# Kernel tuning notes

Measured on AMD Instinct MI355X. Metric: run time of the kernel, lower is better.

Reference implementation:

```python
import jax, jax.numpy as jnp
import numpy as np

N = 100000
E = 1600000
D = 128

def setup_inputs() -> dict:
    key = jax.random.key(0)
    ks = jax.random.split(key, 12)
    s = 1.0 / np.sqrt(D)
    inp = {
        "x": jax.random.normal(ks[0], (N, D), dtype=jnp.float32),
        "edge_index": jax.random.randint(ks[1], (2, E), 0, N, dtype=jnp.int64),
    }
    names = ["Wl1", "bl1", "Wr1", "Wl2", "bl2", "Wr2", "Wl3", "bl3", "Wr3"]
    shapes = [(D, D), (D,), (D, D)] * 3
    for i, (nm, sh) in enumerate(zip(names, shapes)):
        inp[nm] = jax.random.uniform(ks[2 + i], sh, dtype=jnp.float32, minval=-s, maxval=s)
    return inp


def _sage(x, src, dst, Wl, bl, Wr):
    # messages: gather source node features per edge  [E, D]
    msg = x[src]
    agg = jax.ops.segment_sum(msg, dst, num_segments=x.shape[0])  # [N, D]
    cnt = jax.ops.segment_sum(jnp.ones((src.shape[0], 1), x.dtype), dst,
                              num_segments=x.shape[0])            # [N, 1]
    mean = agg / jnp.maximum(cnt, 1.0)
    # PyG SAGEConv: lin_l(mean_neighbors) + lin_r(self); lin_l has bias
    return mean @ Wl.T + bl + x @ Wr.T


def reference(x, edge_index, Wl1, bl1, Wr1, Wl2, bl2, Wr2, Wl3, bl3, Wr3):
    src, dst = edge_index[0], edge_index[1]
    h = jax.nn.relu(_sage(x, src, dst, Wl1, bl1, Wr1))
    h = jax.nn.relu(_sage(h, src, dst, Wl2, bl2, Wr2))
    h = jax.nn.relu(_sage(h, src, dst, Wl3, bl3, Wr3))
    return h
```

## Files before the change

kernel.cpp:

```cpp
#include <hip/hip_runtime.h>
#include <hip/hip_bf16.h>


#define D 128
#define PAD 48
#define NB_SHIFT 8
#define BCAP 5120
#define BIN_CHUNK 4096

typedef __attribute__((ext_vector_type(8))) short bf16x8v;
typedef __attribute__((ext_vector_type(4))) float f32x4v;

#if defined(__has_builtin)
#if __has_builtin(__builtin_amdgcn_raw_buffer_load_b32) && __has_builtin(__builtin_amdgcn_make_buffer_rsrc)
#define USE_BUFLOAD 1
#endif
#endif

__device__ __forceinline__ unsigned short f2b(float f) {
    unsigned u = __float_as_uint(f);
    unsigned r = u + 0x7fffu + ((u >> 16) & 1u);
    return (unsigned short)(r >> 16);
}
__device__ __forceinline__ unsigned pk2(float a, float b) {
    return ((unsigned)f2b(b) << 16) | (unsigned)f2b(a);
}
__device__ __forceinline__ float b2f_lo(unsigned v) { return __uint_as_float(v << 16); }
__device__ __forceinline__ float b2f_hi(unsigned v) { return __uint_as_float(v & 0xffff0000u); }


__global__ void cast_kernel(const float2* __restrict__ in, unsigned* __restrict__ out, int n2) {
    int i = blockIdx.x * blockDim.x + threadIdx.x;
    if (i < n2) { float2 v = in[i]; out[i] = pk2(v.x, v.y); }
}

__global__ void castW_kernel(const float2* __restrict__ w0, const float2* __restrict__ w1,
                             const float2* __restrict__ w2, const float2* __restrict__ w3,
                             const float2* __restrict__ w4, const float2* __restrict__ w5,
                             unsigned* __restrict__ out, int n2each) {
    int i = blockIdx.x * blockDim.x + threadIdx.x;
    if (i >= n2each) return;
    const float2* w;
    switch (blockIdx.y) {
        case 0: w = w0; break; case 1: w = w1; break; case 2: w = w2; break;
        case 3: w = w3; break; case 4: w = w4; break; default: w = w5; break;
    }
    float2 v = w[i];
    out[(size_t)blockIdx.y * n2each + i] = pk2(v.x, v.y);
}


__global__ void bin_kernel(const int* __restrict__ src, const int* __restrict__ dst,
                           int* __restrict__ gcnt, unsigned* __restrict__ pairBuf,
                           int E, int NB) {
    __shared__ int hist[512];
    __shared__ int cur[512];
    const int tid = threadIdx.x;
    for (int b = tid; b < NB; b += 256) hist[b] = 0;
    __syncthreads();
    const int base = blockIdx.x * BIN_CHUNK;
    int end = base + BIN_CHUNK; if (end > E) end = E;
    for (int i = base + tid; i < end; i += 256)
        atomicAdd(&hist[dst[i] >> NB_SHIFT], 1);
    __syncthreads();
    for (int b = tid; b < NB; b += 256)
        cur[b] = hist[b] ? atomicAdd(&gcnt[b], hist[b]) : 0;
    __syncthreads();
    for (int i = base + tid; i < end; i += 256) {
        int d = dst[i];
        int b = d >> NB_SHIFT;
        int p = atomicAdd(&cur[b], 1);
        if (p < BCAP)
            pairBuf[(size_t)b * BCAP + p] = ((unsigned)(d & 255) << 17) | (unsigned)src[i];
    }
}

__global__ void slot_kernel(const unsigned* __restrict__ pairBuf, const int* __restrict__ gcnt,
                            int* __restrict__ colp, int* __restrict__ cnt, int N, int NB) {
    __shared__ int c[256];
    const int tid = threadIdx.x;
    const int b = blockIdx.x;
    c[tid] = 0;
    __syncthreads();
    int n = gcnt[b]; if (n > BCAP) n = BCAP;
    const unsigned* pb = pairBuf + (size_t)b * BCAP;
    for (int k = tid; k < n; k += 256) {
        unsigned v = pb[k];
        int ldst = (int)(v >> 17);
        int s = (int)(v & 0x1FFFFu);
        int p = atomicAdd(&c[ldst], 1);
        if (p < PAD) colp[(size_t)((b << NB_SHIFT) + ldst) * PAD + p] = s << 8;
    }
    __syncthreads();
    int node = (b << NB_SHIFT) + tid;
    if (node < N) cnt[node] = c[tid];
}


__global__ void agg_kernel(const unsigned* __restrict__ Xb2, const int* __restrict__ cnt,
                           const int* __restrict__ colp, unsigned* __restrict__ Mb2, int N) {
    int gt = blockIdx.x * blockDim.x + threadIdx.x;
    int node = gt >> 6;
    int lane = gt & 63;
    if (node >= N) return;

    int c = cnt[node];
    int cc = c < PAD ? c : PAD;
    const int* lst = colp + (size_t)node * PAD;
    const int lane4 = lane << 2;

#ifdef USE_BUFLOAD
    __amdgpu_buffer_rsrc_t rsrc = __builtin_amdgcn_make_buffer_rsrc(
        (void*)Xb2, (short)0, (int)((unsigned)N * 256u), 0x00020000);
#define GATHER(off) ((unsigned)__builtin_amdgcn_raw_buffer_load_b32(rsrc, (off) + lane4, 0, 0))
#else
#define GATHER(off) (*(const unsigned*)((const char*)Xb2 + (size_t)(unsigned)(off) + (unsigned)lane4))
#endif

    float a0 = 0.f, a1 = 0.f, b0 = 0.f, b1 = 0.f;
    float c0 = 0.f, c1 = 0.f, d0 = 0.f, d1 = 0.f;

    int j = 0;
    const int end8 = cc & ~7;
    const int end4 = cc & ~3;

    for (; j < end8; j += 8) {
        int4 i0 = *(const int4*)(lst + j);
        int4 i1 = *(const int4*)(lst + j + 4);
        unsigned v0 = GATHER(i0.x);
        unsigned v1 = GATHER(i0.y);
        unsigned v2 = GATHER(i0.z);
        unsigned v3 = GATHER(i0.w);
        unsigned v4 = GATHER(i1.x);
        unsigned v5 = GATHER(i1.y);
        unsigned v6 = GATHER(i1.z);
        unsigned v7 = GATHER(i1.w);
        a0 += b2f_lo(v0); a1 += b2f_hi(v0);
        b0 += b2f_lo(v1); b1 += b2f_hi(v1);
        c0 += b2f_lo(v2); c1 += b2f_hi(v2);
        d0 += b2f_lo(v3); d1 += b2f_hi(v3);
        a0 += b2f_lo(v4); a1 += b2f_hi(v4);
        b0 += b2f_lo(v5); b1 += b2f_hi(v5);
        c0 += b2f_lo(v6); c1 += b2f_hi(v6);
        d0 += b2f_lo(v7); d1 += b2f_hi(v7);
    }
    if (j < end4) {
        int4 i0 = *(const int4*)(lst + j);
        unsigned v0 = GATHER(i0.x);
        unsigned v1 = GATHER(i0.y);
        unsigned v2 = GATHER(i0.z);
        unsigned v3 = GATHER(i0.w);
        a0 += b2f_lo(v0); a1 += b2f_hi(v0);
        b0 += b2f_lo(v1); b1 += b2f_hi(v1);
        c0 += b2f_lo(v2); c1 += b2f_hi(v2);
        d0 += b2f_lo(v3); d1 += b2f_hi(v3);
        j += 4;
    }
    for (; j < cc; ++j) {
        unsigned v = GATHER(lst[j]);
        a0 += b2f_lo(v); a1 += b2f_hi(v);
    }
#undef GATHER

    float s0f = (a0 + b0) + (c0 + d0);
    float s1f = (a1 + b1) + (c1 + d1);
    float inv = 1.0f / (float)(c > 0 ? c : 1);
    __builtin_nontemporal_store(pk2(s0f * inv, s1f * inv), &Mb2[(size_t)node * 64 + lane]);
}


__global__ __launch_bounds__(256, 2)
void sage_mfma_kernel(const short* __restrict__ Mb,
                      const short* __restrict__ Xb,
                      const short* __restrict__ Wlb,
                      const short* __restrict__ Wrb,
                      const float* __restrict__ bias,
                      short* __restrict__ outb,
                      float* __restrict__ outf,
                      int out_is_bf16, int N)
{
    __shared__ int4 sW[4096];
    const int tid = threadIdx.x;
    const int wid = tid >> 6;
    const int lane = tid & 63;
    const int col16 = lane & 15;
    const int kgrp = lane >> 4;
    const int nb = blockIdx.x * 128 + wid * 32;

    {
        const int4* Wl4 = (const int4*)Wlb;
        const int4* Wr4 = (const int4*)Wrb;
        #pragma unroll
        for (int i = 0; i < 8; ++i) {
            int idx = tid + (i << 8);
            int row = idx >> 4, ch = idx & 15;
            int slot = (row << 4) + (ch ^ (row & 7));
            sW[slot] = Wl4[idx];
            sW[2048 + slot] = Wr4[idx];
        }
    }

    const int m0 = nb + col16;
    const int m1 = nb + 16 + col16;
    const int m0c = m0 < N ? m0 : N - 1;
    const int m1c = m1 < N ? m1 : N - 1;

    const bf16x8v* Mr0 = (const bf16x8v*)(Mb + (size_t)m0c * D);
    const bf16x8v* Mr1 = (const bf16x8v*)(Mb + (size_t)m1c * D);
    const bf16x8v* Xr0 = (const bf16x8v*)(Xb + (size_t)m0c * D);
    const bf16x8v* Xr1 = (const bf16x8v*)(Xb + (size_t)m1c * D);

    bf16x8v aM0[4], aM1[4], aX0[4], aX1[4];
    #pragma unroll
    for (int kc = 0; kc < 4; ++kc) {
        int ci = (kc << 2) + kgrp;
        aM0[kc] = __builtin_nontemporal_load(&Mr0[ci]);
        aM1[kc] = __builtin_nontemporal_load(&Mr1[ci]);
        aX0[kc] = __builtin_nontemporal_load(&Xr0[ci]);
        aX1[kc] = __builtin_nontemporal_load(&Xr1[ci]);
    }

    __syncthreads();

    const float4* bias4 = (const float4*)bias;

    for (int j = 0; j < 8; ++j) {
        f32x4v acc0 = {0.f, 0.f, 0.f, 0.f};
        f32x4v acc1 = {0.f, 0.f, 0.f, 0.f};
        const int wrow = (j << 4) + col16;
        const int rbase = (wrow << 4);
        const int rx = wrow & 7;
        #pragma unroll
        for (int kc = 0; kc < 4; ++kc) {
            int ch = (kc << 2) + kgrp;
            bf16x8v b = *(const bf16x8v*)&sW[rbase + (ch ^ rx)];
            acc0 = __builtin_amdgcn_mfma_f32_16x16x32_bf16(b, aM0[kc], acc0, 0, 0, 0);
            acc1 = __builtin_amdgcn_mfma_f32_16x16x32_bf16(b, aM1[kc], acc1, 0, 0, 0);
        }
        #pragma unroll
        for (int kc = 0; kc < 4; ++kc) {
            int ch = (kc << 2) + kgrp;
            bf16x8v b = *(const bf16x8v*)&sW[2048 + rbase + (ch ^ rx)];
            acc0 = __builtin_amdgcn_mfma_f32_16x16x32_bf16(b, aX0[kc], acc0, 0, 0, 0);
            acc1 = __builtin_amdgcn_mfma_f32_16x16x32_bf16(b, aX1[kc], acc1, 0, 0, 0);
        }
        const int o0 = (j << 4) + (kgrp << 2);
        float4 bv = bias4[(j << 2) + kgrp];
        float v0 = acc0[0] + bv.x, v1 = acc0[1] + bv.y;
        float v2 = acc0[2] + bv.z, v3 = acc0[3] + bv.w;
        float w0 = acc1[0] + bv.x, w1 = acc1[1] + bv.y;
        float w2 = acc1[2] + bv.z, w3 = acc1[3] + bv.w;
        v0 = v0 > 0.f ? v0 : 0.f; v1 = v1 > 0.f ? v1 : 0.f;
        v2 = v2 > 0.f ? v2 : 0.f; v3 = v3 > 0.f ? v3 : 0.f;
        w0 = w0 > 0.f ? w0 : 0.f; w1 = w1 > 0.f ? w1 : 0.f;
        w2 = w2 > 0.f ? w2 : 0.f; w3 = w3 > 0.f ? w3 : 0.f;
        if (out_is_bf16) {
            uint2 p0 = make_uint2(pk2(v0, v1), pk2(v2, v3));
            uint2 p1 = make_uint2(pk2(w0, w1), pk2(w2, w3));
            if (m0 < N) *(uint2*)(outb + (size_t)m0 * D + o0) = p0;
            if (m1 < N) *(uint2*)(outb + (size_t)m1 * D + o0) = p1;
        } else {
            f32x4v p0 = {v0, v1, v2, v3};
            f32x4v p1 = {w0, w1, w2, w3};
            if (m0 < N) __builtin_nontemporal_store(p0, (f32x4v*)(outf + (size_t)m0 * D + o0));
            if (m1 < N) __builtin_nontemporal_store(p1, (f32x4v*)(outf + (size_t)m1 * D + o0));
        }
    }
}


extern "C" void kernel_launch(void* const* d_in, const int* in_sizes, int n_in,
                              void* d_out, int out_size, void* d_ws, size_t ws_size,
                              hipStream_t stream) {
    const float* x   = (const float*)d_in[0];
    const int*   ei  = (const int*)d_in[1];
    const float* Wl1 = (const float*)d_in[2];
    const float* bl1 = (const float*)d_in[3];
    const float* Wr1 = (const float*)d_in[4];
    const float* Wl2 = (const float*)d_in[5];
    const float* bl2 = (const float*)d_in[6];
    const float* Wr2 = (const float*)d_in[7];
    const float* Wl3 = (const float*)d_in[8];
    const float* bl3 = (const float*)d_in[9];
    const float* Wr3 = (const float*)d_in[10];

    const int N = in_sizes[0] / D;
    const int E = in_sizes[1] / 2;
    const int* src = ei;
    const int* dst = ei + E;
    const int NB = (N + 255) >> NB_SHIFT;

    const size_t featB = (size_t)N * D * sizeof(short);
    char* p = (char*)d_ws;
    short* Mb = (short*)p;            p += featB;
    short* Ab = (short*)p;            p += featB;
    short* Bb = (short*)p;            p += featB;
    short* Wb = (short*)p;            p += 6 * 16384 * sizeof(short);
    int* cnt  = (int*)p;              p += (size_t)N * sizeof(int);
    int* colp = (int*)p;              p += (size_t)N * PAD * sizeof(int);
    int* gcnt = (int*)p;              p += (size_t)512 * sizeof(int);
    unsigned* pairBuf = (unsigned*)p;
    float* out = (float*)d_out;

    const int xn2 = N * (D / 2);
    cast_kernel<<<(xn2 + 255) / 256, 256, 0, stream>>>((const float2*)x, (unsigned*)Ab, xn2);
    const int wn2 = (D * D) / 2;
    dim3 wg((wn2 + 255) / 256, 6);
    castW_kernel<<<wg, 256, 0, stream>>>((const float2*)Wl1, (const float2*)Wr1,
                                         (const float2*)Wl2, (const float2*)Wr2,
                                         (const float2*)Wl3, (const float2*)Wr3,
                                         (unsigned*)Wb, wn2);
    const short* Wlb1 = Wb;             const short* Wrb1 = Wb + 16384;
    const short* Wlb2 = Wb + 2 * 16384; const short* Wrb2 = Wb + 3 * 16384;
    const short* Wlb3 = Wb + 4 * 16384; const short* Wrb3 = Wb + 5 * 16384;

    (void)hipMemsetAsync(gcnt, 0, (size_t)NB * sizeof(int), stream);
    const int binBlocks = (E + BIN_CHUNK - 1) / BIN_CHUNK;
    bin_kernel<<<binBlocks, 256, 0, stream>>>(src, dst, gcnt, pairBuf, E, NB);
    slot_kernel<<<NB, 256, 0, stream>>>(pairBuf, gcnt, colp, cnt, N, NB);

    const int aggBlocks  = (int)(((size_t)N * 64 + 255) / 256);
    const int sageBlocks = (N + 127) / 128;

    agg_kernel<<<aggBlocks, 256, 0, stream>>>((const unsigned*)Ab, cnt, colp, (unsigned*)Mb, N);
    sage_mfma_kernel<<<sageBlocks, 256, 0, stream>>>(Mb, Ab, Wlb1, Wrb1, bl1, Bb, nullptr, 1, N);
    agg_kernel<<<aggBlocks, 256, 0, stream>>>((const unsigned*)Bb, cnt, colp, (unsigned*)Mb, N);
    sage_mfma_kernel<<<sageBlocks, 256, 0, stream>>>(Mb, Bb, Wlb2, Wrb2, bl2, Ab, nullptr, 1, N);
    agg_kernel<<<aggBlocks, 256, 0, stream>>>((const unsigned*)Ab, cnt, colp, (unsigned*)Mb, N);
    sage_mfma_kernel<<<sageBlocks, 256, 0, stream>>>(Mb, Ab, Wlb3, Wrb3, bl3, nullptr, out, 0, N);
}
```

Before: 323.9 us.

## Fuse neighbor aggregation into SAGE MFMA kernel via shared-memory mean tile

Merges the gather/mean aggregation kernel with the MFMA linear kernel. Each 512-thread block aggregates 64 nodes into a swizzled LDS tile and then runs the matmul from LDS. This drops the Mb global round trip and three launches per forward. In exchange, each wave aggregates 8 nodes serially, and the weight staging plus LDS use may limit occupancy during the latency-bound gather phase. The cnt int4 loads near N also read past the end of the array without a guard.

```diff
diff --git a/kernel.cpp b/kernel.cpp
--- a/kernel.cpp
+++ b/kernel.cpp
@@ -7,6 +7,7 @@
 #define NB_SHIFT 8
 #define BCAP 5120
 #define BIN_CHUNK 4096
+#define FBLK 64
 
 typedef __attribute__((ext_vector_type(8))) short bf16x8v;
 typedef __attribute__((ext_vector_type(4))) float f32x4v;
@@ -97,102 +98,30 @@
 }
 
 
-__global__ void agg_kernel(const unsigned* __restrict__ Xb2, const int* __restrict__ cnt,
-                           const int* __restrict__ colp, unsigned* __restrict__ Mb2, int N) {
-    int gt = blockIdx.x * blockDim.x + threadIdx.x;
-    int node = gt >> 6;
-    int lane = gt & 63;
-    if (node >= N) return;
-
-    int c = cnt[node];
-    int cc = c < PAD ? c : PAD;
-    const int* lst = colp + (size_t)node * PAD;
-    const int lane4 = lane << 2;
-
-#ifdef USE_BUFLOAD
-    __amdgpu_buffer_rsrc_t rsrc = __builtin_amdgcn_make_buffer_rsrc(
-        (void*)Xb2, (short)0, (int)((unsigned)N * 256u), 0x00020000);
-#define GATHER(off) ((unsigned)__builtin_amdgcn_raw_buffer_load_b32(rsrc, (off) + lane4, 0, 0))
-#else
-#define GATHER(off) (*(const unsigned*)((const char*)Xb2 + (size_t)(unsigned)(off) + (unsigned)lane4))
-#endif
-
-    float a0 = 0.f, a1 = 0.f, b0 = 0.f, b1 = 0.f;
-    float c0 = 0.f, c1 = 0.f, d0 = 0.f, d1 = 0.f;
-
-    int j = 0;
-    const int end8 = cc & ~7;
-    const int end4 = cc & ~3;
-
-    for (; j < end8; j += 8) {
-        int4 i0 = *(const int4*)(lst + j);
-        int4 i1 = *(const int4*)(lst + j + 4);
-        unsigned v0 = GATHER(i0.x);
-        unsigned v1 = GATHER(i0.y);
-        unsigned v2 = GATHER(i0.z);
-        unsigned v3 = GATHER(i0.w);
-        unsigned v4 = GATHER(i1.x);
-        unsigned v5 = GATHER(i1.y);
-        unsigned v6 = GATHER(i1.z);
-        unsigned v7 = GATHER(i1.w);
-        a0 += b2f_lo(v0); a1 += b2f_hi(v0);
-        b0 += b2f_lo(v1); b1 += b2f_hi(v1);
-        c0 += b2f_lo(v2); c1 += b2f_hi(v2);
-        d0 += b2f_lo(v3); d1 += b2f_hi(v3);
-        a0 += b2f_lo(v4); a1 += b2f_hi(v4);
-        b0 += b2f_lo(v5); b1 += b2f_hi(v5);
-        c0 += b2f_lo(v6); c1 += b2f_hi(v6);
-        d0 += b2f_lo(v7); d1 += b2f_hi(v7);
-    }
-    if (j < end4) {
-        int4 i0 = *(const int4*)(lst + j);
-        unsigned v0 = GATHER(i0.x);
-        unsigned v1 = GATHER(i0.y);
-        unsigned v2 = GATHER(i0.z);
-        unsigned v3 = GATHER(i0.w);
-        a0 += b2f_lo(v0); a1 += b2f_hi(v0);
-        b0 += b2f_lo(v1); b1 += b2f_hi(v1);
-        c0 += b2f_lo(v2); c1 += b2f_hi(v2);
-        d0 += b2f_lo(v3); d1 += b2f_hi(v3);
-        j += 4;
-    }
-    for (; j < cc; ++j) {
-        unsigned v = GATHER(lst[j]);
-        a0 += b2f_lo(v); a1 += b2f_hi(v);
-    }
-#undef GATHER
-
-    float s0f = (a0 + b0) + (c0 + d0);
-    float s1f = (a1 + b1) + (c1 + d1);
-    float inv = 1.0f / (float)(c > 0 ? c : 1);
-    __builtin_nontemporal_store(pk2(s0f * inv, s1f * inv), &Mb2[(size_t)node * 64 + lane]);
-}
-
-
-__global__ __launch_bounds__(256, 2)
-void sage_mfma_kernel(const short* __restrict__ Mb,
-                      const short* __restrict__ Xb,
-                      const short* __restrict__ Wlb,
-                      const short* __restrict__ Wrb,
-                      const float* __restrict__ bias,
-                      short* __restrict__ outb,
-                      float* __restrict__ outf,
-                      int out_is_bf16, int N)
+__global__ __launch_bounds__(512, 4)
+void fused_sage_kernel(const short* __restrict__ Xb,
+                       const int* __restrict__ cnt,
+                       const int* __restrict__ colp,
+                       const short* __restrict__ Wlb,
+                       const short* __restrict__ Wrb,
+                       const float* __restrict__ bias,
+                       short* __restrict__ outb,
+                       float* __restrict__ outf,
+                       int out_is_bf16, int N)
 {
     __shared__ int4 sW[4096];
+    __shared__ int4 sM[1024];
     const int tid = threadIdx.x;
     const int wid = tid >> 6;
     const int lane = tid & 63;
-    const int col16 = lane & 15;
-    const int kgrp = lane >> 4;
-    const int nb = blockIdx.x * 128 + wid * 32;
+    const int nb = blockIdx.x * FBLK;
 
     {
         const int4* Wl4 = (const int4*)Wlb;
         const int4* Wr4 = (const int4*)Wrb;
         #pragma unroll
-        for (int i = 0; i < 8; ++i) {
-            int idx = tid + (i << 8);
+        for (int i = 0; i < 4; ++i) {
+            int idx = tid + (i << 9);
             int row = idx >> 4, ch = idx & 15;
             int slot = (row << 4) + (ch ^ (row & 7));
             sW[slot] = Wl4[idx];
@@ -200,70 +129,134 @@
         }
     }
 
-    const int m0 = nb + col16;
-    const int m1 = nb + 16 + col16;
+    const int base = nb + (wid << 3);
+    const int lane4 = lane << 2;
+
+#ifdef USE_BUFLOAD
+    __amdgpu_buffer_rsrc_t rsrc = __builtin_amdgcn_make_buffer_rsrc(
+        (void*)Xb, (short)0, (int)((unsigned)N * 256u), 0x00020000);
+#define GATHER(off) ((unsigned)__builtin_amdgcn_raw_buffer_load_b32(rsrc, (off) + lane4, 0, 0))
+#else
+#define GATHER(off) (*(const unsigned*)((const char*)Xb + (size_t)(unsigned)(off) + (unsigned)lane4))
+#endif
+
+    int4 cA = *(const int4*)(cnt + base);
+    int4 cB = *(const int4*)(cnt + base + 4);
+    int cs[8] = {cA.x, cA.y, cA.z, cA.w, cB.x, cB.y, cB.z, cB.w};
+
+    #pragma unroll 1
+    for (int i = 0; i < 8; ++i) {
+        int node = base + i;
+        if (node >= N) break;
+        int c = cs[i];
+        int cc = c < PAD ? c : PAD;
+        const int* lst = colp + (size_t)node * PAD;
+
+        float a0 = 0.f, a1 = 0.f, b0 = 0.f, b1 = 0.f;
+        float c0 = 0.f, c1 = 0.f, d0 = 0.f, d1 = 0.f;
+        int j = 0;
+        const int end8 = cc & ~7;
+        const int end4 = cc & ~3;
+        for (; j < end8; j += 8) {
+            int4 i0 = *(const int4*)(lst + j);
+            int4 i1 = *(const int4*)(lst + j + 4);
+            unsigned v0 = GATHER(i0.x);
+            unsigned v1 = GATHER(i0.y);
+            unsigned v2 = GATHER(i0.z);
+            unsigned v3 = GATHER(i0.w);
+            unsigned v4 = GATHER(i1.x);
+            unsigned v5 = GATHER(i1.y);
+            unsigned v6 = GATHER(i1.z);
+            unsigned v7 = GATHER(i1.w);
+            a0 += b2f_lo(v0); a1 += b2f_hi(v0);
+            b0 += b2f_lo(v1); b1 += b2f_hi(v1);
+            c0 += b2f_lo(v2); c1 += b2f_hi(v2);
+            d0 += b2f_lo(v3); d1 += b2f_hi(v3);
+            a0 += b2f_lo(v4); a1 += b2f_hi(v4);
+            b0 += b2f_lo(v5); b1 += b2f_hi(v5);
+            c0 += b2f_lo(v6); c1 += b2f_hi(v6);
+            d0 += b2f_lo(v7); d1 += b2f_hi(v7);
+        }
+        if (j < end4) {
+            int4 i0 = *(const int4*)(lst + j);
+            unsigned v0 = GATHER(i0.x);
+            unsigned v1 = GATHER(i0.y);
+            unsigned v2 = GATHER(i0.z);
+            unsigned v3 = GATHER(i0.w);
+            a0 += b2f_lo(v0); a1 += b2f_hi(v0);
+            b0 += b2f_lo(v1); b1 += b2f_hi(v1);
+            c0 += b2f_lo(v2); c1 += b2f_hi(v2);
+            d0 += b2f_lo(v3); d1 += b2f_hi(v3);
+            j += 4;
+        }
+        for (; j < cc; ++j) {
+            unsigned v = GATHER(lst[j]);
+            a0 += b2f_lo(v); a1 += b2f_hi(v);
+        }
+
+        float s0f = (a0 + b0) + (c0 + d0);
+        float s1f = (a1 + b1) + (c1 + d1);
+        float inv = 1.0f / (float)(c > 0 ? c : 1);
+        int nl = node - nb;
+        int slot = (nl << 4) + ((lane >> 2) ^ (nl & 7));
+        ((unsigned*)&sM[slot])[lane & 3] = pk2(s0f * inv, s1f * inv);
+    }
+#undef GATHER
+
+    __syncthreads();
+
+    const int t = wid >> 1;
+    const int h = wid & 1;
+    const int col16 = lane & 15;
+    const int kgrp = lane >> 4;
+
+    const int m0 = nb + (t << 4) + col16;
     const int m0c = m0 < N ? m0 : N - 1;
-    const int m1c = m1 < N ? m1 : N - 1;
-
-    const bf16x8v* Mr0 = (const bf16x8v*)(Mb + (size_t)m0c * D);
-    const bf16x8v* Mr1 = (const bf16x8v*)(Mb + (size_t)m1c * D);
     const bf16x8v* Xr0 = (const bf16x8v*)(Xb + (size_t)m0c * D);
-    const bf16x8v* Xr1 = (const bf16x8v*)(Xb + (size_t)m1c * D);
-
-    bf16x8v aM0[4], aM1[4], aX0[4], aX1[4];
+
+    bf16x8v aX[4], aM[4];
+    const int nl = (t << 4) + col16;
     #pragma unroll
     for (int kc = 0; kc < 4; ++kc) {
-        int ci = (kc << 2) + kgrp;
-        aM0[kc] = __builtin_nontemporal_load(&Mr0[ci]);
-        aM1[kc] = __builtin_nontemporal_load(&Mr1[ci]);
-        aX0[kc] = __builtin_nontemporal_load(&Xr0[ci]);
-        aX1[kc] = __builtin_nontemporal_load(&Xr1[ci]);
-    }
-
-    __syncthreads();
+        int ch = (kc << 2) + kgrp;
+        aX[kc] = __builtin_nontemporal_load(&Xr0[ch]);
+        aM[kc] = *(const bf16x8v*)&sM[(nl << 4) + (ch ^ (nl & 7))];
+    }
 
     const float4* bias4 = (const float4*)bias;
 
-    for (int j = 0; j < 8; ++j) {
-        f32x4v acc0 = {0.f, 0.f, 0.f, 0.f};
-        f32x4v acc1 = {0.f, 0.f, 0.f, 0.f};
-        const int wrow = (j << 4) + col16;
+    #pragma unroll
+    for (int j = 0; j < 4; ++j) {
+        f32x4v acc = {0.f, 0.f, 0.f, 0.f};
+        const int wrow = (h << 6) + (j << 4) + col16;
         const int rbase = (wrow << 4);
         const int rx = wrow & 7;
         #pragma unroll
         for (int kc = 0; kc < 4; ++kc) {
             int ch = (kc << 2) + kgrp;
             bf16x8v b = *(const bf16x8v*)&sW[rbase + (ch ^ rx)];
-            acc0 = __builtin_amdgcn_mfma_f32_16x16x32_bf16(b, aM0[kc], acc0, 0, 0, 0);
-            acc1 = __builtin_amdgcn_mfma_f32_16x16x32_bf16(b, aM1[kc], acc1, 0, 0, 0);
+            acc = __builtin_amdgcn_mfma_f32_16x16x32_bf16(b, aM[kc], acc, 0, 0, 0);
         }
         #pragma unroll
         for (int kc = 0; kc < 4; ++kc) {
             int ch = (kc << 2) + kgrp;
             bf16x8v b = *(const bf16x8v*)&sW[2048 + rbase + (ch ^ rx)];
-            acc0 = __builtin_amdgcn_mfma_f32_16x16x32_bf16(b, aX0[kc], acc0, 0, 0, 0);
-            acc1 = __builtin_amdgcn_mfma_f32_16x16x32_bf16(b, aX1[kc], acc1, 0, 0, 0);
-        }
-        const int o0 = (j << 4) + (kgrp << 2);
-        float4 bv = bias4[(j << 2) + kgrp];
-        float v0 = acc0[0] + bv.x, v1 = acc0[1] + bv.y;
-        float v2 = acc0[2] + bv.z, v3 = acc0[3] + bv.w;
-        float w0 = acc1[0] + bv.x, w1 = acc1[1] + bv.y;
-        float w2 = acc1[2] + bv.z, w3 = acc1[3] + bv.w;
+            acc = __builtin_amdgcn_mfma_f32_16x16x32_bf16(b, aX[kc], acc, 0, 0, 0);
+        }
+        const int o0 = (h << 6) + (j << 4) + (kgrp << 2);
+        float4 bv = bias4[o0 >> 2];
+        float v0 = acc[0] + bv.x, v1 = acc[1] + bv.y;
+        float v2 = acc[2] + bv.z, v3 = acc[3] + bv.w;
         v0 = v0 > 0.f ? v0 : 0.f; v1 = v1 > 0.f ? v1 : 0.f;
         v2 = v2 > 0.f ? v2 : 0.f; v3 = v3 > 0.f ? v3 : 0.f;
-        w0 = w0 > 0.f ? w0 : 0.f; w1 = w1 > 0.f ? w1 : 0.f;
-        w2 = w2 > 0.f ? w2 : 0.f; w3 = w3 > 0.f ? w3 : 0.f;
-        if (out_is_bf16) {
-            uint2 p0 = make_uint2(pk2(v0, v1), pk2(v2, v3));
-            uint2 p1 = make_uint2(pk2(w0, w1), pk2(w2, w3));
-            if (m0 < N) *(uint2*)(outb + (size_t)m0 * D + o0) = p0;
-            if (m1 < N) *(uint2*)(outb + (size_t)m1 * D + o0) = p1;
-        } else {
-            f32x4v p0 = {v0, v1, v2, v3};
-            f32x4v p1 = {w0, w1, w2, w3};
-            if (m0 < N) __builtin_nontemporal_store(p0, (f32x4v*)(outf + (size_t)m0 * D + o0));
-            if (m1 < N) __builtin_nontemporal_store(p1, (f32x4v*)(outf + (size_t)m1 * D + o0));
+        if (m0 < N) {
+            if (out_is_bf16) {
+                uint2 p0 = make_uint2(pk2(v0, v1), pk2(v2, v3));
+                *(uint2*)(outb + (size_t)m0 * D + o0) = p0;
+            } else {
+                f32x4v p0 = {v0, v1, v2, v3};
+                __builtin_nontemporal_store(p0, (f32x4v*)(outf + (size_t)m0 * D + o0));
+            }
         }
     }
 }
@@ -292,7 +285,6 @@
 
     const size_t featB = (size_t)N * D * sizeof(short);
     char* p = (char*)d_ws;
-    short* Mb = (short*)p;            p += featB;
     short* Ab = (short*)p;            p += featB;
     short* Bb = (short*)p;            p += featB;
     short* Wb = (short*)p;            p += 6 * 16384 * sizeof(short);
@@ -319,13 +311,12 @@
     bin_kernel<<<binBlocks, 256, 0, stream>>>(src, dst, gcnt, pairBuf, E, NB);
     slot_kernel<<<NB, 256, 0, stream>>>(pairBuf, gcnt, colp, cnt, N, NB);
 
-    const int aggBlocks  = (int)(((size_t)N * 64 + 255) / 256);
-    const int sageBlocks = (N + 127) / 128;
-
-    agg_kernel<<<aggBlocks, 256, 0, stream>>>((const unsigned*)Ab, cnt, colp, (unsigned*)Mb, N);
-    sage_mfma_kernel<<<sageBlocks, 256, 0, stream>>>(Mb, Ab, Wlb1, Wrb1, bl1, Bb, nullptr, 1, N);
-    agg_kernel<<<aggBlocks, 256, 0, stream>>>((const unsigned*)Bb, cnt, colp, (unsigned*)Mb, N);
-    sage_mfma_kernel<<<sageBlocks, 256, 0, stream>>>(Mb, Bb, Wlb2, Wrb2, bl2, Ab, nullptr, 1, N);
-    agg_kernel<<<aggBlocks, 256, 0, stream>>>((const unsigned*)Ab, cnt, colp, (unsigned*)Mb, N);
-    sage_mfma_kernel<<<sageBlocks, 256, 0, stream>>>(Mb, Ab, Wlb3, Wrb3, bl3, nullptr, out, 0, N);
-}
+    const int fusedBlocks = (N + FBLK - 1) / FBLK;
+
+    fused_sage_kernel<<<fusedBlocks, 512, 0, stream>>>(Ab, cnt, colp, Wlb1, Wrb1,
+                                                       bl1, Bb, nullptr, 1, N);
+    fused_sage_kernel<<<fusedBlocks, 512, 0, stream>>>(Bb, cnt, colp, Wlb2, Wrb2,
+                                                       bl2, Ab, nullptr, 1, N);
+    fused_sage_kernel<<<fusedBlocks, 512, 0, stream>>>(Ab, cnt, colp, Wlb3, Wrb3,
+                                                       bl3, nullptr, out, 0, N);
+}
```

New measurement: 430.1 us. 1.33x slower.
